# Optimization experiments

Hardware: AMD Instinct MI355X
Metric: run time of the kernel (lower is better)

## Reference

```python
import jax, jax.numpy as jnp
import numpy as np

B, S, D = 16, 577, 768
H = 12
DH = D // H  # 64


def setup_inputs() -> dict:
    key = jax.random.key(0)
    ks = jax.random.split(key, 7)
    s = 0.02
    return {
        "hidden_states": jax.random.normal(ks[0], (B, S, D), dtype=jnp.float32),
        "wq": jax.random.normal(ks[1], (D, D), dtype=jnp.float32) * s,
        "bq": jnp.zeros((D,), dtype=jnp.float32),
        "wk": jax.random.normal(ks[2], (D, D), dtype=jnp.float32) * s,
        "bk": jnp.zeros((D,), dtype=jnp.float32),
        "wv": jax.random.normal(ks[3], (D, D), dtype=jnp.float32) * s,
        "bv": jnp.zeros((D,), dtype=jnp.float32),
    }


def reference(hidden_states, wq, bq, wk, bk, wv, bv):
    # Linear projections (torch nn.Linear: x @ W^T + b)
    q = hidden_states @ wq.T + bq  # [B,S,D]
    k = hidden_states @ wk.T + bk
    v = hidden_states @ wv.T + bv

    def split_heads(x):
        return x.reshape(B, S, H, DH).transpose(0, 2, 1, 3)  # [B,H,S,DH]

    q, k, v = split_heads(q), split_heads(k), split_heads(v)
    scale = 1.0 / jnp.sqrt(jnp.float32(DH))
    scores = jnp.einsum("bhqd,bhkd->bhqk", q, k) * scale  # [B,H,S,S]
    probs = jax.nn.softmax(scores, axis=-1)
    ctx = jnp.einsum("bhqk,bhkd->bhqd", probs, v)  # [B,H,S,DH]
    ctx = ctx.transpose(0, 2, 1, 3).reshape(B, S, D)
    return ctx, probs
```

## Files before the change

### kernel.cpp

```cpp
#include <hip/hip_runtime.h>
#include <hip/hip_bf16.h>
#include <cstdint>

#define B_  16
#define S_  577
#define D_  768
#define H_  12
#define SP  640
#define M_  (B_*S_)
#define MP  9344
#define N_  2304
#define SCS 664
#define QSCALE 0.18033688011112042f

typedef __attribute__((ext_vector_type(8))) short short8;
typedef __attribute__((ext_vector_type(4))) float f32x4;

static __device__ __forceinline__ unsigned short f2bf(float f) {
    uint32_t u = __builtin_bit_cast(uint32_t, f);
    uint32_t r = u + 0x7fffu + ((u >> 16) & 1u);
    return (unsigned short)(r >> 16);
}
static __device__ __forceinline__ float bf2f(unsigned short u) {
    uint32_t x = ((uint32_t)u) << 16;
    return __builtin_bit_cast(float, x);
}
static __device__ __forceinline__ float exp2_raw(float x) {
    float r;
    asm("v_exp_f32 %0, %1" : "=v"(r) : "v"(x));
    return r;
}

typedef unsigned int u32;
typedef __attribute__((address_space(3))) u32 lds_u32;
typedef __attribute__((address_space(1))) const u32 gbl_u32;
static __device__ __forceinline__ void gll16(const void* g, void* l) {
    __builtin_amdgcn_global_load_lds((gbl_u32*)g, (lds_u32*)l, 16, 0, 0);
}


__global__ __launch_bounds__(256) void prep(
    const float* __restrict__ X,
    const float* __restrict__ Wq, const float* __restrict__ Wk, const float* __restrict__ Wv,
    unsigned short* __restrict__ Xb, unsigned short* __restrict__ Wb,
    unsigned short* __restrict__ Vf)
{
    const int NT1 = MP * 192;
    const int NT2 = N_ * 192;
    const int VPAD = 192 * 1024;
    const int total = NT1 + NT2 + VPAD;
    const int stride = gridDim.x * 256;
    for (int i = blockIdx.x * 256 + threadIdx.x; i < total; i += stride) {
        if (i < NT1) {
            int row = i / 192, c4 = i - row * 192;
            uint2 out = make_uint2(0u, 0u);
            if (row < M_) {
                float4 v = *(const float4*)(X + (size_t)row * 768 + c4 * 4);
                unsigned short p[4] = { f2bf(v.x), f2bf(v.y), f2bf(v.z), f2bf(v.w) };
                out = *(uint2*)p;
            }
            *(uint2*)(Xb + (size_t)row * 768 + c4 * 4) = out;
        } else if (i < NT1 + NT2) {
            int j = i - NT1;
            int row = j / 192, c4 = j - row * 192;
            const float* src = (row < 768) ? (Wq + (size_t)row * 768)
                             : (row < 1536) ? (Wk + (size_t)(row - 768) * 768)
                                            : (Wv + (size_t)(row - 1536) * 768);
            float4 v = *(const float4*)(src + c4 * 4);
            unsigned short p[4] = { f2bf(v.x), f2bf(v.y), f2bf(v.z), f2bf(v.w) };
            *(uint2*)(Wb + (size_t)row * 768 + c4 * 4) = *(uint2*)p;
        } else {
            int j = i - NT1 - NT2;
            int bh = j >> 10, rem = j & 1023;
            *(uint2*)(Vf + (size_t)bh * 40960 + 36864 + rem * 4) = make_uint2(0u, 0u);
        }
    }
}

__global__ __launch_bounds__(256) void qkv_gemm(
    const unsigned short* __restrict__ Xb, const unsigned short* __restrict__ Wb,
    const float* __restrict__ bq, const float* __restrict__ bk, const float* __restrict__ bv,
    unsigned short* __restrict__ Qf, unsigned short* __restrict__ Kf,
    unsigned short* __restrict__ Vf)
{
    __shared__ unsigned short Als[128 * 64];
    __shared__ unsigned short Bls[128 * 64];

    const int bid = blockIdx.x;
    int mt, nt;
    if (bid < 1296) {
        const int xcd = bid & 7, sq = bid >> 3;
        mt = xcd * 9 + sq / 18;
        nt = sq % 18;
    } else {
        mt = 72;
        nt = bid - 1296;
    }

    const bool qk = (nt < 12);
    const int tid = threadIdx.x, lane = tid & 63, wid = tid >> 6;
    const int wm = wid >> 1, wn = wid & 1;
    const int m0 = mt * 128, n0 = nt * 128;
    const int l15 = lane & 15, g = lane >> 4;
    const int prow = lane >> 3, pc8 = lane & 7;

    const unsigned short* Pa = qk ? Bls : Als;
    const unsigned short* Pb = qk ? Als : Bls;

    f32x4 acc[4][4] = {};

    for (int kk = 0; kk < 768; kk += 64) {
        __syncthreads();
        #pragma unroll
        for (int t = 0; t < 4; ++t) {
            int row  = wid * 32 + t * 8 + prow;
            int scol = ((pc8 ^ (row & 7)) * 8);
            gll16(Xb + (size_t)(m0 + row) * 768 + kk + scol, &Als[(wid * 32 + t * 8) * 64]);
            gll16(Wb + (size_t)(n0 + row) * 768 + kk + scol, &Bls[(wid * 32 + t * 8) * 64]);
        }
        __syncthreads();

        #pragma unroll
        for (int ks = 0; ks < 2; ++ks) {
            short8 fa[4], fb[4];
            #pragma unroll
            for (int i = 0; i < 4; ++i) {
                int row = wm * 64 + i * 16 + l15;
                fa[i] = *(const short8*)&Pa[row * 64 + (((ks * 4 + g) ^ (row & 7)) * 8)];
            }
            #pragma unroll
            for (int j = 0; j < 4; ++j) {
                int row = wn * 64 + j * 16 + l15;
                fb[j] = *(const short8*)&Pb[row * 64 + (((ks * 4 + g) ^ (row & 7)) * 8)];
            }
            #pragma unroll
            for (int i = 0; i < 4; ++i)
                #pragma unroll
                for (int j = 0; j < 4; ++j)
                    acc[i][j] = __builtin_amdgcn_mfma_f32_16x16x32_bf16(fa[i], fb[j], acc[i][j], 0, 0, 0);
        }
    }

    if (qk) {
        const float* bb = (nt < 6) ? bq : bk;
        unsigned short* Dst = (nt < 6) ? Qf : Kf;
        const float scale = (nt < 6) ? QSCALE : 1.0f;
        #pragma unroll
        for (int i = 0; i < 4; ++i) {
            int nrow0 = n0 - ((nt < 6) ? 0 : 768) + wm * 64 + i * 16 + g * 4;
            float4 b4 = *(const float4*)(bb + nrow0);
            int hh = nrow0 >> 6, d0 = nrow0 & 63;
            int dh5 = d0 >> 5;
            int dsub = ((d0 >> 3) & 3) * 8 + (d0 & 7);
            #pragma unroll
            for (int j = 0; j < 4; ++j) {
                int m = m0 + wn * 64 + j * 16 + l15;
                if (m >= M_) continue;
                int b = m / 577, s = m - b * 577;
                unsigned short p[4];
                p[0] = f2bf((acc[i][j][0] + b4.x) * scale);
                p[1] = f2bf((acc[i][j][1] + b4.y) * scale);
                p[2] = f2bf((acc[i][j][2] + b4.z) * scale);
                p[3] = f2bf((acc[i][j][3] + b4.w) * scale);
                size_t off;
                if (nt < 6)
                    off = (((size_t)(b * 40 + (s >> 4)) * 12 + hh) * 2 + dh5) * 512
                        + (s & 15) * 32 + dsub;
                else
                    off = ((((size_t)(b * 12 + hh)) * 10 + (s >> 6)) * 8 + ((s >> 4) & 3) * 2 + dh5) * 512
                        + (s & 15) * 32 + dsub;
                *(uint2*)(Dst + off) = *(uint2*)p;
            }
        }
    } else {
        #pragma unroll
        for (int j = 0; j < 4; ++j) {
            int n = n0 + wn * 64 + j * 16 + l15;
            int nn = n - 1536;
            float bias = bv[nn];
            int hh = nn >> 6, dwh = nn & 63;
            #pragma unroll
            for (int i = 0; i < 4; ++i) {
                #pragma unroll
                for (int r = 0; r < 4; ++r) {
                    int m = m0 + wm * 64 + i * 16 + g * 4 + r;
                    if (m >= M_) continue;
                    int b = m / 577, s = m - b * 577;
                    float val = acc[i][j][r] + bias;
                    size_t off = (((size_t)(b * 12 + hh) * 20 + (s >> 5)) * 4 + (dwh >> 4)) * 512
                               + (dwh & 15) * 32 + ((s >> 3) & 3) * 8 + (s & 7);
                    Vf[off] = f2bf(val);
                }
            }
        }
    }
}

__global__ __launch_bounds__(256) void attn(
    const unsigned short* __restrict__ Qf, const unsigned short* __restrict__ Kf,
    const unsigned short* __restrict__ Vf,
    float* __restrict__ ctx, float* __restrict__ probs)
{
    __shared__ unsigned short sc[16 * SCS];
    __shared__ float rowinv[16];

    const int wg  = blockIdx.x;
    const int idx = (wg & 7) * 888 + (wg >> 3);
    const int bh  = idx / 37;
    const int qt  = idx - bh * 37;
    const int h   = bh % 12, b = bh / 12;

    const int tid = threadIdx.x, lane = tid & 63, wid = tid >> 6;
    const int l15 = lane & 15, g = lane >> 4;
    const int q0 = qt * 16;
    const int lofs = l15 * 32 + g * 8;
    const int r = tid >> 4, c0 = tid & 15;

    const unsigned short* qb = Qf + ((size_t)(b * 40 + qt) * 12 + h) * 1024 + lofs;
    short8 aq0 = *(const short8*)qb;
    short8 aq1 = *(const short8*)(qb + 512);

    const unsigned short* kb0 = Kf + (size_t)bh * 40960 + wid * 1024 + lofs;
    #pragma unroll
    for (int c = 0; c < 10; ++c) {
        const unsigned short* kb = kb0 + c * 4096;
        short8 bk0 = *(const short8*)kb;
        short8 bk1 = *(const short8*)(kb + 512);
        f32x4 s4 = {};
        s4 = __builtin_amdgcn_mfma_f32_16x16x32_bf16(aq0, bk0, s4, 0, 0, 0);
        s4 = __builtin_amdgcn_mfma_f32_16x16x32_bf16(aq1, bk1, s4, 0, 0, 0);
        int key = c * 64 + wid * 16 + l15;
        #pragma unroll
        for (int rr = 0; rr < 4; ++rr)
            sc[(g * 4 + rr) * SCS + key] = (key < S_) ? f2bf(s4[rr]) : (unsigned short)0xFF80u;
    }
    __syncthreads();

    unsigned short* rowp = &sc[r * SCS];
    float inv;
    {
        short8 v[5];
        float m = -1e30f;
        #pragma unroll
        for (int i = 0; i < 5; ++i) {
            v[i] = *(const short8*)&rowp[(c0 + 16 * i) * 8];
            #pragma unroll
            for (int jj = 0; jj < 8; ++jj) m = fmaxf(m, bf2f((unsigned short)v[i][jj]));
        }
        #pragma unroll
        for (int o = 8; o; o >>= 1) m = fmaxf(m, __shfl_xor(m, o));

        float ssum = 0.f;
        #pragma unroll
        for (int i = 0; i < 5; ++i) {
            short8 w;
            #pragma unroll
            for (int jj = 0; jj < 8; ++jj) {
                float e = exp2_raw(bf2f((unsigned short)v[i][jj]) - m);
                ssum += e;
                w[jj] = (short)f2bf(e);
            }
            *(short8*)&rowp[(c0 + 16 * i) * 8] = w;
        }
        #pragma unroll
        for (int o = 8; o; o >>= 1) ssum += __shfl_xor(ssum, o);
        inv = 1.0f / ssum;
        if (c0 == 0) rowinv[r] = inv;
    }
    __syncthreads();

    {
        int q = q0 + r;
        if (q < S_) {
            float* prow = probs + ((size_t)bh * S_ + q) * S_;
            #pragma unroll
            for (int i = 0; i < 5; ++i) {
                int ch = c0 + 16 * i;
                short8 v = *(const short8*)&rowp[ch * 8];
                if (ch < 72) {
                    f32x4 o0, o1;
                    o0[0] = bf2f((unsigned short)v[0]) * inv; o0[1] = bf2f((unsigned short)v[1]) * inv;
                    o0[2] = bf2f((unsigned short)v[2]) * inv; o0[3] = bf2f((unsigned short)v[3]) * inv;
                    o1[0] = bf2f((unsigned short)v[4]) * inv; o1[1] = bf2f((unsigned short)v[5]) * inv;
                    o1[2] = bf2f((unsigned short)v[6]) * inv; o1[3] = bf2f((unsigned short)v[7]) * inv;
                    __builtin_nontemporal_store(o0, (f32x4*)&prow[ch * 8]);
                    __builtin_nontemporal_store(o1, (f32x4*)&prow[ch * 8 + 4]);
                } else if (ch == 72) {
                    __builtin_nontemporal_store(bf2f((unsigned short)v[0]) * inv, &prow[576]);
                }
            }
        }
    }

    f32x4 oc = {};
    const unsigned short* vb0 = Vf + (size_t)bh * 40960 + wid * 512 + lofs;
    const unsigned short* pb  = &sc[l15 * SCS + g * 8];
    #pragma unroll
    for (int kk = 0; kk < 20; ++kk) {
        short8 ap = *(const short8*)(pb + kk * 32);
        short8 bv = *(const short8*)(vb0 + kk * 2048);
        oc = __builtin_amdgcn_mfma_f32_16x16x32_bf16(ap, bv, oc, 0, 0, 0);
    }
    #pragma unroll
    for (int rr = 0; rr < 4; ++rr) {
        int qr = g * 4 + rr;
        int qq = q0 + qr;
        if (qq < S_)
            __builtin_nontemporal_store(oc[rr] * rowinv[qr],
                &ctx[((size_t)b * S_ + qq) * D_ + h * 64 + wid * 16 + l15]);
    }
}

extern "C" void kernel_launch(void* const* d_in, const int* in_sizes, int n_in,
                              void* d_out, int out_size, void* d_ws, size_t ws_size,
                              hipStream_t stream) {
    const float* X  = (const float*)d_in[0];
    const float* Wq = (const float*)d_in[1];
    const float* bq = (const float*)d_in[2];
    const float* Wk = (const float*)d_in[3];
    const float* bk = (const float*)d_in[4];
    const float* Wv = (const float*)d_in[5];
    const float* bv = (const float*)d_in[6];

    float* ctx   = (float*)d_out;
    float* probs = ctx + (size_t)B_ * S_ * D_;

    unsigned short* Xb = (unsigned short*)probs;
    unsigned short* Wb = Xb + (size_t)MP * 768;

    unsigned short* Qf = (unsigned short*)d_ws;
    unsigned short* Kf = Qf + (size_t)7864320;
    unsigned short* Vf = Kf + (size_t)7864320;

    prep<<<dim3(1024), 256, 0, stream>>>(X, Wq, Wk, Wv, Xb, Wb, Vf);
    qkv_gemm<<<dim3(1314), 256, 0, stream>>>(Xb, Wb, bq, bk, bv, Qf, Kf, Vf);
    attn<<<dim3(7104), 256, 0, stream>>>(Qf, Kf, Vf, ctx, probs);
}
```

Baseline: 211.3 us.

## Use hardware bf16 conversion, hoist epilogue index math, split PV accumulators

Replaces the manual round-to-nearest bf16 conversion with the compiler's native __bf16 cast, packing pairs so it can map to packed conversion instructions. Precomputes the scatter address terms in the QKV GEMM epilogue so the per-element div/mod and offset math is hoisted out of the inner loops. In attention, the softmax reloads rows from LDS instead of holding them in registers and uses tree reductions. The PV MFMA chain is split into two independent accumulators to break the dependency chain, and launch bounds are raised to request higher occupancy. These changes cost extra LDS reads and may cause register spills under the tighter occupancy bound.

```diff
diff --git a/kernel.cpp b/kernel.cpp
--- a/kernel.cpp
+++ b/kernel.cpp
@@ -15,11 +15,14 @@
 
 typedef __attribute__((ext_vector_type(8))) short short8;
 typedef __attribute__((ext_vector_type(4))) float f32x4;
+typedef unsigned int u32;
 
 static __device__ __forceinline__ unsigned short f2bf(float f) {
-    uint32_t u = __builtin_bit_cast(uint32_t, f);
-    uint32_t r = u + 0x7fffu + ((u >> 16) & 1u);
-    return (unsigned short)(r >> 16);
+    __bf16 b = (__bf16)f;
+    return __builtin_bit_cast(unsigned short, b);
+}
+static __device__ __forceinline__ u32 cvtpk(float lo, float hi) {
+    return (u32)f2bf(lo) | ((u32)f2bf(hi) << 16);
 }
 static __device__ __forceinline__ float bf2f(unsigned short u) {
     uint32_t x = ((uint32_t)u) << 16;
@@ -31,7 +34,6 @@
     return r;
 }
 
-typedef unsigned int u32;
 typedef __attribute__((address_space(3))) u32 lds_u32;
 typedef __attribute__((address_space(1))) const u32 gbl_u32;
 static __device__ __forceinline__ void gll16(const void* g, void* l) {
@@ -56,8 +58,7 @@
             uint2 out = make_uint2(0u, 0u);
             if (row < M_) {
                 float4 v = *(const float4*)(X + (size_t)row * 768 + c4 * 4);
-                unsigned short p[4] = { f2bf(v.x), f2bf(v.y), f2bf(v.z), f2bf(v.w) };
-                out = *(uint2*)p;
+                out.x = cvtpk(v.x, v.y); out.y = cvtpk(v.z, v.w);
             }
             *(uint2*)(Xb + (size_t)row * 768 + c4 * 4) = out;
         } else if (i < NT1 + NT2) {
@@ -67,8 +68,9 @@
                              : (row < 1536) ? (Wk + (size_t)(row - 768) * 768)
                                             : (Wv + (size_t)(row - 1536) * 768);
             float4 v = *(const float4*)(src + c4 * 4);
-            unsigned short p[4] = { f2bf(v.x), f2bf(v.y), f2bf(v.z), f2bf(v.w) };
-            *(uint2*)(Wb + (size_t)row * 768 + c4 * 4) = *(uint2*)p;
+            uint2 out;
+            out.x = cvtpk(v.x, v.y); out.y = cvtpk(v.z, v.w);
+            *(uint2*)(Wb + (size_t)row * 768 + c4 * 4) = out;
         } else {
             int j = i - NT1 - NT2;
             int bh = j >> 10, rem = j & 1023;
@@ -145,58 +147,64 @@
         const float* bb = (nt < 6) ? bq : bk;
         unsigned short* Dst = (nt < 6) ? Qf : Kf;
         const float scale = (nt < 6) ? QSCALE : 1.0f;
+        const int n0p = n0 - ((nt < 6) ? 0 : 768);
+
+        float4 b4[4]; int Pi[4];
         #pragma unroll
         for (int i = 0; i < 4; ++i) {
-            int nrow0 = n0 - ((nt < 6) ? 0 : 768) + wm * 64 + i * 16 + g * 4;
-            float4 b4 = *(const float4*)(bb + nrow0);
+            int nrow0 = n0p + wm * 64 + i * 16 + g * 4;
+            b4[i] = *(const float4*)(bb + nrow0);
             int hh = nrow0 >> 6, d0 = nrow0 & 63;
-            int dh5 = d0 >> 5;
-            int dsub = ((d0 >> 3) & 3) * 8 + (d0 & 7);
-            #pragma unroll
-            for (int j = 0; j < 4; ++j) {
-                int m = m0 + wn * 64 + j * 16 + l15;
-                if (m >= M_) continue;
-                int b = m / 577, s = m - b * 577;
-                unsigned short p[4];
-                p[0] = f2bf((acc[i][j][0] + b4.x) * scale);
-                p[1] = f2bf((acc[i][j][1] + b4.y) * scale);
-                p[2] = f2bf((acc[i][j][2] + b4.z) * scale);
-                p[3] = f2bf((acc[i][j][3] + b4.w) * scale);
-                size_t off;
-                if (nt < 6)
-                    off = (((size_t)(b * 40 + (s >> 4)) * 12 + hh) * 2 + dh5) * 512
-                        + (s & 15) * 32 + dsub;
-                else
-                    off = ((((size_t)(b * 12 + hh)) * 10 + (s >> 6)) * 8 + ((s >> 4) & 3) * 2 + dh5) * 512
-                        + (s & 15) * 32 + dsub;
-                *(uint2*)(Dst + off) = *(uint2*)p;
+            int base = (d0 >> 5) * 512 + ((d0 >> 3) & 3) * 8 + (d0 & 7);
+            Pi[i] = ((nt < 6) ? hh * 1024 : hh * 40960) + base;
+        }
+        #pragma unroll
+        for (int j = 0; j < 4; ++j) {
+            int m = m0 + wn * 64 + j * 16 + l15;
+            if (m >= M_) continue;
+            int b = m / 577, s = m - b * 577;
+            int Pj = (nt < 6)
+                   ? b * 491520 + (s >> 4) * 12288 + (s & 15) * 32
+                   : b * 491520 + (s >> 6) * 4096 + ((s >> 4) & 3) * 1024 + (s & 15) * 32;
+            #pragma unroll
+            for (int i = 0; i < 4; ++i) {
+                uint2 p;
+                p.x = cvtpk((acc[i][j][0] + b4[i].x) * scale, (acc[i][j][1] + b4[i].y) * scale);
+                p.y = cvtpk((acc[i][j][2] + b4[i].z) * scale, (acc[i][j][3] + b4[i].w) * scale);
+                *(uint2*)(Dst + Pj + Pi[i]) = p;
             }
         }
     } else {
+        int Pir[4][4]; bool mv[4][4];
+        #pragma unroll
+        for (int i = 0; i < 4; ++i) {
+            int mi = m0 + wm * 64 + i * 16 + g * 4;
+            int b = mi / 577, s = mi - b * 577;
+            #pragma unroll
+            for (int r = 0; r < 4; ++r) {
+                int bb2 = b, ss = s + r;
+                if (ss >= 577) { bb2++; ss -= 577; }
+                mv[i][r] = (mi + r < M_);
+                Pir[i][r] = bb2 * 491520 + (ss >> 5) * 2048 + ((ss >> 3) & 3) * 8 + (ss & 7);
+            }
+        }
         #pragma unroll
         for (int j = 0; j < 4; ++j) {
-            int n = n0 + wn * 64 + j * 16 + l15;
-            int nn = n - 1536;
+            int nn = n0 + wn * 64 + j * 16 + l15 - 1536;
             float bias = bv[nn];
             int hh = nn >> 6, dwh = nn & 63;
-            #pragma unroll
-            for (int i = 0; i < 4; ++i) {
+            int Pn = hh * 40960 + (dwh >> 4) * 512 + (dwh & 15) * 32;
+            #pragma unroll
+            for (int i = 0; i < 4; ++i)
                 #pragma unroll
-                for (int r = 0; r < 4; ++r) {
-                    int m = m0 + wm * 64 + i * 16 + g * 4 + r;
-                    if (m >= M_) continue;
-                    int b = m / 577, s = m - b * 577;
-                    float val = acc[i][j][r] + bias;
-                    size_t off = (((size_t)(b * 12 + hh) * 20 + (s >> 5)) * 4 + (dwh >> 4)) * 512
-                               + (dwh & 15) * 32 + ((s >> 3) & 3) * 8 + (s & 7);
-                    Vf[off] = f2bf(val);
-                }
-            }
-        }
-    }
-}
-
-__global__ __launch_bounds__(256) void attn(
+                for (int r = 0; r < 4; ++r)
+                    if (mv[i][r])
+                        Vf[Pn + Pir[i][r]] = f2bf(acc[i][j][r] + bias);
+        }
+    }
+}
+
+__global__ __launch_bounds__(256, 7) void attn(
     const unsigned short* __restrict__ Qf, const unsigned short* __restrict__ Kf,
     const unsigned short* __restrict__ Vf,
     float* __restrict__ ctx, float* __restrict__ probs)
@@ -239,13 +247,15 @@
     unsigned short* rowp = &sc[r * SCS];
     float inv;
     {
-        short8 v[5];
         float m = -1e30f;
         #pragma unroll
         for (int i = 0; i < 5; ++i) {
-            v[i] = *(const short8*)&rowp[(c0 + 16 * i) * 8];
-            #pragma unroll
-            for (int jj = 0; jj < 8; ++jj) m = fmaxf(m, bf2f((unsigned short)v[i][jj]));
+            short8 v = *(const short8*)&rowp[(c0 + 16 * i) * 8];
+            float t0 = fmaxf(bf2f((unsigned short)v[0]), bf2f((unsigned short)v[1]));
+            float t1 = fmaxf(bf2f((unsigned short)v[2]), bf2f((unsigned short)v[3]));
+            float t2 = fmaxf(bf2f((unsigned short)v[4]), bf2f((unsigned short)v[5]));
+            float t3 = fmaxf(bf2f((unsigned short)v[6]), bf2f((unsigned short)v[7]));
+            m = fmaxf(m, fmaxf(fmaxf(t0, t1), fmaxf(t2, t3)));
         }
         #pragma unroll
         for (int o = 8; o; o >>= 1) m = fmaxf(m, __shfl_xor(m, o));
@@ -253,14 +263,20 @@
         float ssum = 0.f;
         #pragma unroll
         for (int i = 0; i < 5; ++i) {
-            short8 w;
-            #pragma unroll
-            for (int jj = 0; jj < 8; ++jj) {
-                float e = exp2_raw(bf2f((unsigned short)v[i][jj]) - m);
-                ssum += e;
-                w[jj] = (short)f2bf(e);
-            }
-            *(short8*)&rowp[(c0 + 16 * i) * 8] = w;
+            short8 v = *(const short8*)&rowp[(c0 + 16 * i) * 8];
+            float e0 = exp2_raw(bf2f((unsigned short)v[0]) - m);
+            float e1 = exp2_raw(bf2f((unsigned short)v[1]) - m);
+            float e2 = exp2_raw(bf2f((unsigned short)v[2]) - m);
+            float e3 = exp2_raw(bf2f((unsigned short)v[3]) - m);
+            float e4 = exp2_raw(bf2f((unsigned short)v[4]) - m);
+            float e5 = exp2_raw(bf2f((unsigned short)v[5]) - m);
+            float e6 = exp2_raw(bf2f((unsigned short)v[6]) - m);
+            float e7 = exp2_raw(bf2f((unsigned short)v[7]) - m);
+            uint4 w;
+            w.x = cvtpk(e0, e1); w.y = cvtpk(e2, e3);
+            w.z = cvtpk(e4, e5); w.w = cvtpk(e6, e7);
+            *(uint4*)&rowp[(c0 + 16 * i) * 8] = w;
+            ssum += ((e0 + e1) + (e2 + e3)) + ((e4 + e5) + (e6 + e7));
         }
         #pragma unroll
         for (int o = 8; o; o >>= 1) ssum += __shfl_xor(ssum, o);
@@ -292,15 +308,19 @@
         }
     }
 
-    f32x4 oc = {};
+    f32x4 oc0 = {}, oc1 = {};
     const unsigned short* vb0 = Vf + (size_t)bh * 40960 + wid * 512 + lofs;
     const unsigned short* pb  = &sc[l15 * SCS + g * 8];
     #pragma unroll
-    for (int kk = 0; kk < 20; ++kk) {
-        short8 ap = *(const short8*)(pb + kk * 32);
-        short8 bv = *(const short8*)(vb0 + kk * 2048);
-        oc = __builtin_amdgcn_mfma_f32_16x16x32_bf16(ap, bv, oc, 0, 0, 0);
-    }
+    for (int kk = 0; kk < 20; kk += 2) {
+        short8 ap0 = *(const short8*)(pb + kk * 32);
+        short8 bv0 = *(const short8*)(vb0 + (size_t)kk * 2048);
+        oc0 = __builtin_amdgcn_mfma_f32_16x16x32_bf16(ap0, bv0, oc0, 0, 0, 0);
+        short8 ap1 = *(const short8*)(pb + (kk + 1) * 32);
+        short8 bv1 = *(const short8*)(vb0 + (size_t)(kk + 1) * 2048);
+        oc1 = __builtin_amdgcn_mfma_f32_16x16x32_bf16(ap1, bv1, oc1, 0, 0, 0);
+    }
+    f32x4 oc = oc0 + oc1;
     #pragma unroll
     for (int rr = 0; rr < 4; ++rr) {
         int qr = g * 4 + rr;
```

Measured after the change: 210.0 us. Within noise of the previous version (-0.6%).
